# Performance work log

Measured on AMD Instinct MI355X. Metric: run time of the kernel, lower is better.

## Reference

```python
import jax, jax.numpy as jnp
import numpy as np

DIM = 256
B = 8
H = 56
W = 56
K = 2
EPS = 1e-5  # torch BatchNorm2d default eps


def _conv1x1(x, w, b):
    # x: [B,C,H,W], w: [O,C], b: [O]
    return jnp.einsum('oc,bchw->bohw', w, x) + b[None, :, None, None]


def _bn(x, g, be, m, v):
    # inference-mode BatchNorm2d with running stats
    s = g / jnp.sqrt(v + EPS)
    return x * s[None, :, None, None] + (be - m * s)[None, :, None, None]


def _grapher(x, w1, b1, g1, be1, m1, v1, wg, bg, gg, beg, mg, vg, w2, b2, g2, be2, m2, v2):
    # fc1: 1x1 conv + BN
    h = _bn(_conv1x1(x, w1, b1), g1, be1, m1, v1)
    Hh, Ww = h.shape[2], h.shape[3]
    # MRConv4d: running max over circular-shift differences
    # torch.cat([x[:,:,-i:,:], x[:,:,:-i,:]], dim=2) == jnp.roll(x, i, axis=2)
    xj = jnp.zeros_like(h)

    def body_h(c, i):
        return jnp.maximum(c, h - jnp.roll(h, i, axis=2)), None

    xj, _ = jax.lax.scan(body_h, xj, jnp.arange(K, Hh, K))

    def body_w(c, i):
        return jnp.maximum(c, h - jnp.roll(h, i, axis=3)), None

    xj, _ = jax.lax.scan(body_w, xj, jnp.arange(K, Ww, K))

    cat = jnp.concatenate([h, xj], axis=1)  # [B, 2*dim, H, W]
    # MRConv4d.nn: Conv2d(2*dim, 2*dim, 1) -> BN(2*dim) -> GELU (exact erf)
    g = jax.nn.gelu(_bn(_conv1x1(cat, wg, bg), gg, beg, mg, vg), approximate=False)
    # fc2: Conv2d(2*dim, dim, 1) + BN(dim), then residual
    return _bn(_conv1x1(g, w2, b2), g2, be2, m2, v2) + x


def setup_inputs() -> dict:
    key = jax.random.key(0)
    ks = jax.random.split(key, 12)
    d, d2 = DIM, 2 * DIM

    def w(k, o, c):
        return jax.random.normal(k, (o, c), jnp.float32) * np.float32(1.0 / np.sqrt(c))

    return {
        'x': jax.random.normal(ks[0], (B, d, H, W), jnp.float32),
        'w1': w(ks[1], d, d), 'b1': jnp.zeros((d,), jnp.float32),
        'g1': jnp.ones((d,), jnp.float32), 'be1': jnp.zeros((d,), jnp.float32),
        'm1': jax.random.normal(ks[2], (d,), jnp.float32) * 0.1,
        'v1': jax.random.uniform(ks[3], (d,), jnp.float32, 0.5, 1.5),
        'wg': w(ks[4], d2, d2), 'bg': jnp.zeros((d2,), jnp.float32),
        'gg': jnp.ones((d2,), jnp.float32), 'beg': jnp.zeros((d2,), jnp.float32),
        'mg': jax.random.normal(ks[5], (d2,), jnp.float32) * 0.1,
        'vg': jax.random.uniform(ks[6], (d2,), jnp.float32, 0.5, 1.5),
        'w2': w(ks[7], d, d2), 'b2': jnp.zeros((d,), jnp.float32),
        'g2': jnp.ones((d,), jnp.float32), 'be2': jnp.zeros((d,), jnp.float32),
        'm2': jax.random.normal(ks[8], (d,), jnp.float32) * 0.1,
        'v2': jax.random.uniform(ks[9], (d,), jnp.float32, 0.5, 1.5),
    }


def reference(x, w1, b1, g1, be1, m1, v1, wg, bg, gg, beg, mg, vg, w2, b2, g2, be2, m2, v2):
    return _grapher(x, w1, b1, g1, be1, m1, v1, wg, bg, gg, beg, mg, vg, w2, b2, g2, be2, m2, v2)
```

## Files before the change

### kernel.cpp

```cpp
#include <hip/hip_runtime.h>
#include <math.h>

#define SPB 3136
#define NB 8
#define MTOT (NB*SPB)
#define EPS 1e-5f
#define XT_LD  288
#define CAT_LD 544

typedef unsigned short u16;
typedef __attribute__((ext_vector_type(8))) short short8;
typedef __attribute__((ext_vector_type(4))) float float4v;

__device__ __forceinline__ float b2f(u16 v){ unsigned u=((unsigned)v)<<16; float f; __builtin_memcpy(&f,&u,4); return f; }
__device__ __forceinline__ u16 f2b(float f){ unsigned u; __builtin_memcpy(&u,&f,4); u += 0x7fffu + ((u>>16)&1u); return (u16)(u>>16); }
__device__ __forceinline__ float gelu_f(float z){
  float t = 1.5957691216f * z * (1.0f + 0.044715f*z*z);
  return __fdividef(z, 1.0f + __expf(-t));
}

__device__ __forceinline__ void gll16(const u16* g, u16* l){
  __builtin_amdgcn_global_load_lds((const __attribute__((address_space(1))) void*)g,
                                   (__attribute__((address_space(3))) void*)l, 16, 0, 0);
}

__global__ void prep_k(const float* __restrict__ x, u16* __restrict__ xt,
                       const float* __restrict__ w1,const float* __restrict__ wg,const float* __restrict__ w2,
                       const float* b1,const float* g1,const float* be1,const float* m1,const float* v1,
                       const float* bg,const float* gg,const float* beg,const float* mg,const float* vg,
                       const float* b2,const float* g2,const float* be2,const float* m2,const float* v2,
                       u16* __restrict__ w1b,u16* __restrict__ wgb,u16* __restrict__ w2b,float* cst){
  __shared__ float t[32][33];
  if (blockIdx.z < 8) {
    int b = blockIdx.z, ct = blockIdx.y, st = blockIdx.x;
    int ts = threadIdx.x, tc = threadIdx.y;
    #pragma unroll
    for (int i=0;i<4;i++){
      int c = tc + i*8;
      t[c][ts] = x[((size_t)(b*256 + ct*32 + c))*SPB + st*32 + ts];
    }
    __syncthreads();
    #pragma unroll
    for (int i=0;i<4;i++){
      int r = tc + i*8;
      xt[((size_t)(b*SPB + st*32 + r))*XT_LD + ct*32 + ts] = f2b(t[ts][r]);
    }
  } else {
    int tid = threadIdx.y*32 + threadIdx.x;
    int w = ((blockIdx.z-8)*8 + blockIdx.y)*98 + blockIdx.x;
    int i = w*256 + tid;
    if (i < 65536)  w1b[(i>>8)*XT_LD  + (i&255)] = f2b(w1[i]);
    if (i < 262144) wgb[(i>>9)*CAT_LD + (i&511)] = f2b(wg[i]);
    if (i < 131072) w2b[(i>>9)*CAT_LD + (i&511)] = f2b(w2[i]);
    if (i < 256) {
      float s = g1[i]*rsqrtf(v1[i]+EPS);
      cst[i] = s; cst[256+i] = b1[i]*s + be1[i] - m1[i]*s;
      float s2 = g2[i]*rsqrtf(v2[i]+EPS);
      cst[1536+i] = s2; cst[1792+i] = b2[i]*s2 + be2[i] - m2[i]*s2;
    }
    if (i < 512) {
      float s = gg[i]*rsqrtf(vg[i]+EPS);
      cst[512+i] = s; cst[1024+i] = bg[i]*s + beg[i] - mg[i]*s;
    }
  }
}

__global__ __launch_bounds__(256) void minmax_k(const u16* __restrict__ cat, float* __restrict__ rmin, float* __restrict__ cmin){
  __shared__ float red[8][256];
  int b = blockIdx.x/56, i = blockIdx.x%56;
  int col = blockIdx.y;
  int slice = threadIdx.x >> 5;
  int c0 = (threadIdx.x & 31) * 8;
  const u16* base; size_t stride;
  if (!col){ base = cat + ((size_t)(b*SPB + i*56))*CAT_LD + c0; stride = CAT_LD; }
  else     { base = cat + ((size_t)(b*SPB + i))*CAT_LD + c0;    stride = (size_t)56*CAT_LD; }
  float m[8];
  #pragma unroll
  for (int k=0;k<8;k++) m[k]=3.4e38f;
  #pragma unroll
  for (int jj=0;jj<7;jj++){
    short8 v = *(const short8*)(base + (size_t)(slice + jj*8)*stride);
    #pragma unroll
    for (int k=0;k<8;k++) m[k] = fminf(m[k], b2f((u16)v[k]));
  }
  #pragma unroll
  for (int k=0;k<8;k++) red[slice][c0+k] = m[k];
  __syncthreads();
  int t = threadIdx.x;
  if (t < 64){
    int par = t >> 5;
    int cc = (t & 31) * 8;
    float* out = col ? cmin : rmin;
    float* p = &out[((size_t)(b*2+par)*56 + i)*256 + cc];
    #pragma unroll
    for (int k=0;k<8;k++)
      p[k] = fminf(fminf(red[par][cc+k], red[par+2][cc+k]),
                   fminf(red[par+4][cc+k], red[par+6][cc+k]));
  }
}

__global__ __launch_bounds__(256) void xj_k(u16* __restrict__ cat, const float* __restrict__ rmin, const float* __restrict__ cmin){
  int b = blockIdx.y;
  int t = threadIdx.x;
  int s = blockIdx.x*8 + (t>>5);
  int c0 = (t&31)*8;
  int y = s/56, x = s%56;
  size_t idx = ((size_t)(b*SPB + s))*CAT_LD;
  short8 h8 = *(const short8*)&cat[idx + c0];
  const float* cp = &cmin[((size_t)(b*2+(y&1))*56 + x)*256 + c0];
  const float* rp = &rmin[((size_t)(b*2+(x&1))*56 + y)*256 + c0];
  float4v cv0 = *(const float4v*)cp, cv1 = *(const float4v*)(cp+4);
  float4v rv0 = *(const float4v*)rp, rv1 = *(const float4v*)(rp+4);
  short8 o;
  #pragma unroll
  for (int j=0;j<8;j++){
    float cm = (j<4) ? cv0[j] : cv1[j-4];
    float rm = (j<4) ? rv0[j] : rv1[j-4];
    o[j] = (short)f2b(fmaxf(0.0f, b2f((u16)h8[j]) - fminf(cm, rm)));
  }
  *(short8*)&cat[idx + 256 + c0] = o;
}

__device__ __forceinline__ int xcd_remap(int orig, int nwg){
  int q = nwg >> 3, r = nwg & 7, xc = orig & 7, rest = orig >> 3;
  int base = (xc < r) ? xc*(q+1) : r*(q+1) + (xc-r)*q;
  return base + rest;
}

template<int KTOT, int LDA, int LDB, int EPI>
__global__ __launch_bounds__(512,4) void gemm_k(
    const u16* __restrict__ Ain, const u16* __restrict__ Wt,
    const float* __restrict__ scale, const float* __restrict__ bias,
    void* __restrict__ outp, const float* __restrict__ resid)
{
  __shared__ __align__(16) u16 smem[32768];
  const int tid = threadIdx.x;
  const int nwg = gridDim.x * gridDim.y;
  const int flat = blockIdx.y * gridDim.x + blockIdx.x;
  const int s_ = xcd_remap(flat, nwg);
  const int m0 = (s_ / gridDim.y) * 128;
  const int o0 = (s_ % gridDim.y) * 128;
  const int lane = tid & 63, wid = tid >> 6;
  const int quad = lane >> 4, l16 = lane & 15;

  float4v acc[8];
  #pragma unroll
  for (int j=0;j<8;j++) acc[j] = (float4v){0.f,0.f,0.f,0.f};

  const int row8 = tid >> 3;
  const int gc   = ((tid & 7) ^ (row8 & 7)) * 8;
  const u16* ga0 = Ain + ((size_t)(m0 + row8))*LDA + gc;
  const u16* ga1 = ga0 + (size_t)64*LDA;
  const u16* gb0 = Wt  + ((size_t)(o0 + row8))*LDB + gc;
  const u16* gb1 = gb0 + (size_t)64*LDB;
  u16* l8 = smem + tid*8;

  auto STAGE = [&](int kt, int buf){
    u16* b_ = l8 + buf*16384;
    gll16(ga0 + kt, b_);
    gll16(ga1 + kt, b_ + 4096);
    gll16(gb0 + kt, b_ + 8192);
    gll16(gb1 + kt, b_ + 12288);
  };
  const int r7 = l16 & 7;
  auto COMPUTE = [&](int buf){
    const u16* A_ = smem + buf*16384;
    const u16* B_ = A_ + 8192;
    #pragma unroll
    for (int kk=0; kk<2; kk++){
      const int sl = ((kk*4 + quad) ^ r7) * 8;
      short8 af = *(const short8*)&A_[(wid*16 + l16)*64 + sl];
      short8 bfr[8];
      #pragma unroll
      for (int in=0;in<8;in++) bfr[in] = *(const short8*)&B_[(in*16+l16)*64 + sl];
      #pragma unroll
      for (int in=0;in<8;in++)
        acc[in] = __builtin_amdgcn_mfma_f32_16x16x32_bf16(af, bfr[in], acc[in], 0, 0, 0);
    }
  };

  constexpr int NIT = KTOT / 64;
  STAGE(0, 0);
  #pragma unroll
  for (int t = 0; t < NIT; ++t) {
    __builtin_amdgcn_sched_barrier(0);
    asm volatile("s_waitcnt vmcnt(0) lgkmcnt(0)" ::: "memory");
    __builtin_amdgcn_s_barrier();
    __builtin_amdgcn_sched_barrier(0);
    if (t + 1 < NIT) STAGE((t+1)*64, (t+1)&1);
    COMPUTE(t&1);
  }
  __syncthreads();

  if (EPI == 1 || EPI == 2) {
    u16* tile = smem;
    #pragma unroll
    for (int in=0;in<8;in++){
      int ol = in*16 + l16;
      float sc = scale[o0+ol], bi = bias[o0+ol];
      #pragma unroll
      for (int r=0;r<4;r++){
        float v = acc[in][r]*sc + bi;
        if (EPI==2) v = gelu_f(v);
        tile[(wid*16+quad*4+r)*128 + ol] = f2b(v);
      }
    }
    __syncthreads();
    u16* op = (u16*)outp;
    #pragma unroll
    for (int p=0;p<4;p++){
      int chunk = p*512 + tid;
      int rr = chunk >> 4, off = (chunk & 15)*8;
      *(uint4*)&op[((size_t)(m0 + rr))*CAT_LD + o0 + off] = *(const uint4*)&tile[rr*128 + off];
    }
  } else {
    float* ftile = (float*)smem;
    float* op = (float*)outp;
    #pragma unroll
    for (int h=0; h<2; h++){
      #pragma unroll
      for (int in4=0;in4<4;in4++){
        int in = h*4 + in4;
        int c64 = in4*16 + l16;
        int og = o0 + h*64 + c64;
        float sc = scale[og], bi = bias[og];
        float4v v;
        #pragma unroll
        for (int r=0;r<4;r++) v[r] = acc[in][r]*sc + bi;
        *(float4v*)&ftile[c64*132 + wid*16 + quad*4] = v;
      }
      __syncthreads();
      #pragma unroll
      for (int p=0;p<4;p++){
        int chunk = p*512 + tid;
        int rr = chunk >> 5, off = (chunk & 31)*4;
        int m = m0 + off;
        int b = m / SPB, s = m - b*SPB;
        size_t g = ((size_t)(b*256 + o0 + h*64 + rr))*SPB + s;
        float4v v = *(const float4v*)&ftile[rr*132 + off];
        v.x += resid[g]; v.y += resid[g+1]; v.z += resid[g+2]; v.w += resid[g+3];
        *(float4v*)&op[g] = v;
      }
      __syncthreads();
    }
  }
}

extern "C" void kernel_launch(void* const* d_in, const int* in_sizes, int n_in,
                              void* d_out, int out_size, void* d_ws, size_t ws_size,
                              hipStream_t stream)
{
  const float* x  = (const float*)d_in[0];
  const float* w1 = (const float*)d_in[1];
  const float* b1 = (const float*)d_in[2];
  const float* g1 = (const float*)d_in[3];
  const float* be1= (const float*)d_in[4];
  const float* m1 = (const float*)d_in[5];
  const float* v1 = (const float*)d_in[6];
  const float* wg = (const float*)d_in[7];
  const float* bg = (const float*)d_in[8];
  const float* gg = (const float*)d_in[9];
  const float* beg= (const float*)d_in[10];
  const float* mg = (const float*)d_in[11];
  const float* vg = (const float*)d_in[12];
  const float* w2 = (const float*)d_in[13];
  const float* b2 = (const float*)d_in[14];
  const float* g2 = (const float*)d_in[15];
  const float* be2= (const float*)d_in[16];
  const float* m2 = (const float*)d_in[17];
  const float* v2 = (const float*)d_in[18];

  char* ws = (char*)d_ws;
  size_t off = 0;
  auto alloc = [&](size_t bytes){ void* p = ws + off; off += (bytes + 255) & ~(size_t)255; return p; };
  u16* xt    = (u16*)alloc((size_t)MTOT*XT_LD*2);
  u16* catt  = (u16*)alloc((size_t)MTOT*CAT_LD*2);
  u16* gt    = (u16*)alloc((size_t)MTOT*CAT_LD*2);
  u16* w1b   = (u16*)alloc((size_t)256*XT_LD*2);
  u16* wgb   = (u16*)alloc((size_t)512*CAT_LD*2);
  u16* w2b   = (u16*)alloc((size_t)256*CAT_LD*2);
  float* cst = (float*)alloc((size_t)2048*4);
  float* rmin= (float*)alloc((size_t)NB*2*56*256*4);
  float* cmin= (float*)alloc((size_t)NB*2*56*256*4);

  hipLaunchKernelGGL(prep_k, dim3(98,8,10), dim3(32,8), 0, stream,
                     x, xt, w1,wg,w2, b1,g1,be1,m1,v1, bg,gg,beg,mg,vg, b2,g2,be2,m2,v2,
                     w1b,wgb,w2b, cst);
  hipLaunchKernelGGL((gemm_k<256,XT_LD,XT_LD,1>), dim3(196,2), dim3(512), 0, stream,
                     xt, w1b, cst+0, cst+256, (void*)catt, (const float*)nullptr);
  hipLaunchKernelGGL(minmax_k, dim3(NB*56,2), dim3(256), 0, stream, catt, rmin, cmin);
  hipLaunchKernelGGL(xj_k, dim3(392, NB), dim3(256), 0, stream, catt, rmin, cmin);
  hipLaunchKernelGGL((gemm_k<512,CAT_LD,CAT_LD,2>), dim3(196,4), dim3(512), 0, stream,
                     catt, wgb, cst+512, cst+1024, (void*)gt, (const float*)nullptr);
  hipLaunchKernelGGL((gemm_k<512,CAT_LD,CAT_LD,3>), dim3(196,2), dim3(512), 0, stream,
                     gt, w2b, cst+1536, cst+1792, d_out, x);
}
```

Measured before the change: 177.1 us.

## Fuse min-reduction and xj kernels; triple-buffer GEMM K-loop staging

Replaces the separate minmax and xj kernels with one kernel per (batch, 8-channel) slice that loads the whole 56x56 plane into LDS, computes row and column parity minima there, and writes xj. This removes the rmin/cmin global round trip and one launch, but the grid is only 256 blocks and the LDS-column accesses may bank-conflict. Separately, the GEMM moves from double to triple buffering with a partial vmcnt wait so loads run two stages ahead, raising LDS to 96KB and lowering the occupancy hint from 4 to 2.

```diff
diff --git a/kernel.cpp b/kernel.cpp
--- a/kernel.cpp
+++ b/kernel.cpp
@@ -65,60 +65,50 @@
   }
 }
 
-__global__ __launch_bounds__(256) void minmax_k(const u16* __restrict__ cat, float* __restrict__ rmin, float* __restrict__ cmin){
-  __shared__ float red[8][256];
-  int b = blockIdx.x/56, i = blockIdx.x%56;
-  int col = blockIdx.y;
-  int slice = threadIdx.x >> 5;
-  int c0 = (threadIdx.x & 31) * 8;
-  const u16* base; size_t stride;
-  if (!col){ base = cat + ((size_t)(b*SPB + i*56))*CAT_LD + c0; stride = CAT_LD; }
-  else     { base = cat + ((size_t)(b*SPB + i))*CAT_LD + c0;    stride = (size_t)56*CAT_LD; }
-  float m[8];
-  #pragma unroll
-  for (int k=0;k<8;k++) m[k]=3.4e38f;
-  #pragma unroll
-  for (int jj=0;jj<7;jj++){
-    short8 v = *(const short8*)(base + (size_t)(slice + jj*8)*stride);
-    #pragma unroll
-    for (int k=0;k<8;k++) m[k] = fminf(m[k], b2f((u16)v[k]));
-  }
-  #pragma unroll
-  for (int k=0;k<8;k++) red[slice][c0+k] = m[k];
+__global__ __launch_bounds__(448) void hxj_k(u16* __restrict__ cat){
+  __shared__ u16 hl[SPB*8];
+  __shared__ float rowm[56][2][8];
+  __shared__ float colm[56][2][8];
+  const int b = blockIdx.y;
+  const int c0 = blockIdx.x * 8;
+  const int t = threadIdx.x;
+  const size_t base = (size_t)b*SPB*CAT_LD + c0;
+  #pragma unroll
+  for (int i=0;i<7;i++){
+    int s = i*448 + t;
+    *(short8*)&hl[s*8] = *(const short8*)&cat[base + (size_t)s*CAT_LD];
+  }
   __syncthreads();
-  int t = threadIdx.x;
-  if (t < 64){
-    int par = t >> 5;
-    int cc = (t & 31) * 8;
-    float* out = col ? cmin : rmin;
-    float* p = &out[((size_t)(b*2+par)*56 + i)*256 + cc];
-    #pragma unroll
-    for (int k=0;k<8;k++)
-      p[k] = fminf(fminf(red[par][cc+k], red[par+2][cc+k]),
-                   fminf(red[par+4][cc+k], red[par+6][cc+k]));
-  }
-}
-
-__global__ __launch_bounds__(256) void xj_k(u16* __restrict__ cat, const float* __restrict__ rmin, const float* __restrict__ cmin){
-  int b = blockIdx.y;
-  int t = threadIdx.x;
-  int s = blockIdx.x*8 + (t>>5);
-  int c0 = (t&31)*8;
-  int y = s/56, x = s%56;
-  size_t idx = ((size_t)(b*SPB + s))*CAT_LD;
-  short8 h8 = *(const short8*)&cat[idx + c0];
-  const float* cp = &cmin[((size_t)(b*2+(y&1))*56 + x)*256 + c0];
-  const float* rp = &rmin[((size_t)(b*2+(x&1))*56 + y)*256 + c0];
-  float4v cv0 = *(const float4v*)cp, cv1 = *(const float4v*)(cp+4);
-  float4v rv0 = *(const float4v*)rp, rv1 = *(const float4v*)(rp+4);
-  short8 o;
-  #pragma unroll
-  for (int j=0;j<8;j++){
-    float cm = (j<4) ? cv0[j] : cv1[j-4];
-    float rm = (j<4) ? rv0[j] : rv1[j-4];
-    o[j] = (short)f2b(fmaxf(0.0f, b2f((u16)h8[j]) - fminf(cm, rm)));
-  }
-  *(short8*)&cat[idx + 256 + c0] = o;
+  #pragma unroll
+  for (int half=0; half<2; half++){
+    int id = half*448 + t;
+    int a = id >> 4;
+    int par = (id >> 3) & 1;
+    int k = id & 7;
+    float mr = 3.4e38f, mc = 3.4e38f;
+    #pragma unroll
+    for (int j=0;j<28;j++){
+      int u = par + j*2;
+      mr = fminf(mr, b2f(hl[(a*56 + u)*8 + k]));
+      mc = fminf(mc, b2f(hl[(u*56 + a)*8 + k]));
+    }
+    rowm[a][par][k] = mr;
+    colm[a][par][k] = mc;
+  }
+  __syncthreads();
+  #pragma unroll
+  for (int i=0;i<7;i++){
+    int s = i*448 + t;
+    int y = s/56, x = s - y*56;
+    short8 h8 = *(const short8*)&hl[s*8];
+    short8 o;
+    #pragma unroll
+    for (int k=0;k<8;k++){
+      float m = fminf(colm[x][y&1][k], rowm[y][x&1][k]);
+      o[k] = (short)f2b(fmaxf(0.0f, b2f((u16)h8[k]) - m));
+    }
+    *(short8*)&cat[base + (size_t)s*CAT_LD + 256] = o;
+  }
 }
 
 __device__ __forceinline__ int xcd_remap(int orig, int nwg){
@@ -128,12 +118,12 @@
 }
 
 template<int KTOT, int LDA, int LDB, int EPI>
-__global__ __launch_bounds__(512,4) void gemm_k(
+__global__ __launch_bounds__(512,2) void gemm_k(
     const u16* __restrict__ Ain, const u16* __restrict__ Wt,
     const float* __restrict__ scale, const float* __restrict__ bias,
     void* __restrict__ outp, const float* __restrict__ resid)
 {
-  __shared__ __align__(16) u16 smem[32768];
+  __shared__ __align__(16) u16 smem[49152];
   const int tid = threadIdx.x;
   const int nwg = gridDim.x * gridDim.y;
   const int flat = blockIdx.y * gridDim.x + blockIdx.x;
@@ -181,14 +171,16 @@
 
   constexpr int NIT = KTOT / 64;
   STAGE(0, 0);
+  STAGE(64, 1);
   #pragma unroll
   for (int t = 0; t < NIT; ++t) {
     __builtin_amdgcn_sched_barrier(0);
-    asm volatile("s_waitcnt vmcnt(0) lgkmcnt(0)" ::: "memory");
+    if (t + 1 < NIT) asm volatile("s_waitcnt vmcnt(4) lgkmcnt(0)" ::: "memory");
+    else             asm volatile("s_waitcnt vmcnt(0) lgkmcnt(0)" ::: "memory");
     __builtin_amdgcn_s_barrier();
     __builtin_amdgcn_sched_barrier(0);
-    if (t + 1 < NIT) STAGE((t+1)*64, (t+1)&1);
-    COMPUTE(t&1);
+    if (t + 2 < NIT) STAGE((t+2)*64, (t+2)%3);
+    COMPUTE(t%3);
   }
   __syncthreads();
 
@@ -280,16 +272,13 @@
   u16* wgb   = (u16*)alloc((size_t)512*CAT_LD*2);
   u16* w2b   = (u16*)alloc((size_t)256*CAT_LD*2);
   float* cst = (float*)alloc((size_t)2048*4);
-  float* rmin= (float*)alloc((size_t)NB*2*56*256*4);
-  float* cmin= (float*)alloc((size_t)NB*2*56*256*4);
 
   hipLaunchKernelGGL(prep_k, dim3(98,8,10), dim3(32,8), 0, stream,
                      x, xt, w1,wg,w2, b1,g1,be1,m1,v1, bg,gg,beg,mg,vg, b2,g2,be2,m2,v2,
                      w1b,wgb,w2b, cst);
   hipLaunchKernelGGL((gemm_k<256,XT_LD,XT_LD,1>), dim3(196,2), dim3(512), 0, stream,
                      xt, w1b, cst+0, cst+256, (void*)catt, (const float*)nullptr);
-  hipLaunchKernelGGL(minmax_k, dim3(NB*56,2), dim3(256), 0, stream, catt, rmin, cmin);
-  hipLaunchKernelGGL(xj_k, dim3(392, NB), dim3(256), 0, stream, catt, rmin, cmin);
+  hipLaunchKernelGGL(hxj_k, dim3(32, NB), dim3(448), 0, stream, catt);
   hipLaunchKernelGGL((gemm_k<512,CAT_LD,CAT_LD,2>), dim3(196,4), dim3(512), 0, stream,
                      catt, wgb, cst+512, cst+1024, (void*)gt, (const float*)nullptr);
   hipLaunchKernelGGL((gemm_k<512,CAT_LD,CAT_LD,3>), dim3(196,2), dim3(512), 0, stream,
```

New measurement: 205.8 us. 16.2% more time.
